# Kernel optimization log

Hardware: AMD Instinct MI355X
Metric: run time of the kernel (lower is better)

The kernel has to match this reference:

```python
import jax, jax.numpy as jnp
import numpy as np

B, D, U = 8192, 2048, 2048  # batch rows, input dim, units
NB_FACTOR = 3
MASK_DENSITY = 1.0 / 16.0  # butterfly-like sparse factor density


def _glorot_uniform(key, shape):
    fan_in, fan_out = shape[0], shape[-1]
    limit = np.sqrt(6.0 / (fan_in + fan_out)).astype(np.float32)
    return jax.random.uniform(key, shape, jnp.float32, -limit, limit)


def setup_inputs() -> dict:
    key = jax.random.key(0)
    kx, km0, km1, km2, kk0, kk1, kk2, ks = jax.random.split(key, 8)
    x = jax.random.normal(kx, (B, D), jnp.float32)
    # Fixed sparsity patterns (constants, like K.constant sparsity_masks)
    m0 = (jax.random.uniform(km0, (D, U)) < MASK_DENSITY).astype(jnp.float32)
    m1 = (jax.random.uniform(km1, (U, U)) < MASK_DENSITY).astype(jnp.float32)
    m2 = (jax.random.uniform(km2, (U, U)) < MASK_DENSITY).astype(jnp.float32)
    k0 = _glorot_uniform(kk0, (D, U))
    k1 = _glorot_uniform(kk1, (U, U))
    k2 = _glorot_uniform(kk2, (U, U))
    scaling = _glorot_uniform(ks, (1,))  # scaler weight, shape (1,)
    bias = jnp.zeros((U,), jnp.float32)
    return {"x": x, "k0": k0, "k1": k1, "k2": k2,
            "m0": m0, "m1": m1, "m2": m2,
            "scaling": scaling, "bias": bias}


def reference(x, k0, k1, k2, m0, m1, m2, scaling, bias):
    # output = activation(scaling * (x @ (k0*m0) @ (k1*m1) @ (k2*m2)) + bias)
    out = x @ (k0 * m0)          # [B, U]
    out = out @ (k1 * m1)        # [B, U]
    out = out @ (k2 * m2)        # [B, U]
    out = scaling * out + bias   # scale then channels-last bias add
    return jax.nn.relu(out)
```

## Files before the change

### kernel.cpp

```cpp
#include <hip/hip_runtime.h>
#include <hip/hip_bf16.h>


typedef __attribute__((ext_vector_type(8))) short  short8;
typedef __attribute__((ext_vector_type(8))) ushort ushort8v;
typedef __attribute__((ext_vector_type(4))) float  f32x4;

#define KD 2048
#define ND 2048

__device__ __forceinline__ ushort f2b(float f) {
    union { float f; unsigned u; } v; v.f = f;
    unsigned r = v.u + 0x7fffu + ((v.u >> 16) & 1u);
    return (ushort)(r >> 16);
}

__device__ __forceinline__ void gload16(const ushort* g, ushort* l) {
    __builtin_amdgcn_global_load_lds(
        (const __attribute__((address_space(1))) void*)g,
        (__attribute__((address_space(3))) void*)l, 16, 0, 0);
}

__global__ __launch_bounds__(256)
void convx(const float* __restrict__ x, ushort* __restrict__ xb)
{
    const size_t i = (size_t)blockIdx.x * 256 + threadIdx.x;
    const float4* src = reinterpret_cast<const float4*>(x) + i * 2;
    const float4 f0 = src[0], f1 = src[1];
    ushort8v u;
    u[0]=f2b(f0.x); u[1]=f2b(f0.y); u[2]=f2b(f0.z); u[3]=f2b(f0.w);
    u[4]=f2b(f1.x); u[5]=f2b(f1.y); u[6]=f2b(f1.z); u[7]=f2b(f1.w);
    reinterpret_cast<ushort8v*>(xb)[i] = u;
}

__global__ __launch_bounds__(256)
void convT3(const float* __restrict__ k0w, const float* __restrict__ k1w,
            const float* __restrict__ k2w, const float* __restrict__ m0w,
            const float* __restrict__ m1w, const float* __restrict__ m2w,
            ushort* __restrict__ wbT)
{
    const int z = blockIdx.z;
    const float* kw = z == 0 ? k0w : (z == 1 ? k1w : k2w);
    const float* mw = z == 0 ? m0w : (z == 1 ? m1w : m2w);
    ushort* o = wbT + (size_t)z * KD * ND;

    __shared__ ushort t[32][36];
    const int tid = threadIdx.x;
    const int bk = blockIdx.x * 32, bn = blockIdx.y * 32;
    {
        const int r = tid >> 3, c = (tid & 7) * 4;
        const size_t g = (size_t)(bk + r) * ND + bn + c;
        const float4 kv = *reinterpret_cast<const float4*>(kw + g);
        const float4 mv = *reinterpret_cast<const float4*>(mw + g);
        t[r][c + 0] = f2b(kv.x * mv.x);
        t[r][c + 1] = f2b(kv.y * mv.y);
        t[r][c + 2] = f2b(kv.z * mv.z);
        t[r][c + 3] = f2b(kv.w * mv.w);
    }
    __syncthreads();
    {
        const int n = tid >> 3, kq = (tid & 7) * 4;
        ushort4 ov;
        ov.x = t[kq + 0][n]; ov.y = t[kq + 1][n];
        ov.z = t[kq + 2][n]; ov.w = t[kq + 3][n];
        *reinterpret_cast<ushort4*>(&o[(size_t)(bn + n) * KD + bk + kq]) = ov;
    }
}

template<int EPI>
__global__ __launch_bounds__(512, 2)
void gemm256(const ushort* __restrict__ A, const ushort* __restrict__ BT,
             void* __restrict__ Cout,
             const float* __restrict__ scaling, const float* __restrict__ bias)
{
    __shared__ ushort S[2][2][2][256 * 32];

    const int tid  = threadIdx.x;
    const int lane = tid & 63;
    const int wid  = tid >> 6;
    const int wr   = wid >> 2, wc = wid & 3;
    const int l15  = lane & 15;
    const int kq   = lane >> 4;
    const int id   = blockIdx.x;
    const int swz  = (id & 7) * 32 + (id >> 3);
    const int bn   = (swz & 7) * 256;
    const int bm   = (swz >> 3) * 256;
    const int srow = lane >> 2;
    const int wrow = wid * 32;
    const int ssw  = ((lane & 3) ^ ((srow >> 1) & 3)) * 8;
    const int rsw  = (kq ^ ((l15 >> 1) & 3)) * 8;

    f32x4 acc[8][4] = {};

#define STAGE(op, bufl, kh, tile, G, g0) do {                                        \
    gload16(G + (size_t)((g0) + wrow + srow)      * KD + (tile)*64 + (kh)*32 + ssw,  \
            &S[bufl][op][kh][(wrow)      * 32]);                                     \
    gload16(G + (size_t)((g0) + wrow + 16 + srow) * KD + (tile)*64 + (kh)*32 + ssw,  \
            &S[bufl][op][kh][(wrow + 16) * 32]);                                     \
  } while (0)

#define BAR()  asm volatile("s_barrier" ::: "memory")
#define VM6()  asm volatile("s_waitcnt vmcnt(6)" ::: "memory")
#define VM0()  asm volatile("s_waitcnt vmcnt(0)" ::: "memory")
#define LGK0() asm volatile("s_waitcnt lgkmcnt(0)" ::: "memory")
#define SB()   __builtin_amdgcn_sched_barrier(0)
#define PRI1() __builtin_amdgcn_s_setprio(1)
#define PRI0() __builtin_amdgcn_s_setprio(0)

#define FA(bufl, kh, m) (*(const short8*)&S[bufl][0][kh][(wr*128 + (m)*16 + l15)*32 + rsw])
#define FB(bufl, kh, n) (*(const short8*)&S[bufl][1][kh][(wc*64  + (n)*16 + l15)*32 + rsw])

#define MM4(r, av, b0_, b1_, b2_, b3_)                                                \
    acc[r][0] = __builtin_amdgcn_mfma_f32_16x16x32_bf16(b0_, av, acc[r][0], 0, 0, 0); \
    acc[r][1] = __builtin_amdgcn_mfma_f32_16x16x32_bf16(b1_, av, acc[r][1], 0, 0, 0); \
    acc[r][2] = __builtin_amdgcn_mfma_f32_16x16x32_bf16(b2_, av, acc[r][2], 0, 0, 0); \
    acc[r][3] = __builtin_amdgcn_mfma_f32_16x16x32_bf16(b3_, av, acc[r][3], 0, 0, 0)

#define HALFGRP(bufl, ST0, ST1, ST2, ST3, GATE) do {                                  \
    short8 xa0 = FA(bufl,0,0), xa1 = FA(bufl,0,1), xa2 = FA(bufl,0,2), xa3 = FA(bufl,0,3); \
    short8 xb0 = FB(bufl,0,0), xb1 = FB(bufl,0,1), xb2 = FB(bufl,0,2), xb3 = FB(bufl,0,3); \
    ST0; BAR(); SB(); PRI1();                                                         \
    MM4(0, xa0, xb0, xb1, xb2, xb3); MM4(1, xa1, xb0, xb1, xb2, xb3);                 \
    MM4(2, xa2, xb0, xb1, xb2, xb3); MM4(3, xa3, xb0, xb1, xb2, xb3);                 \
    PRI0(); SB(); LGK0(); BAR();                                                      \
    short8 xa4 = FA(bufl,0,4), xa5 = FA(bufl,0,5), xa6 = FA(bufl,0,6), xa7 = FA(bufl,0,7); \
    short8 xc0 = FA(bufl,1,0), xc1 = FA(bufl,1,1), xc2 = FA(bufl,1,2), xc3 = FA(bufl,1,3); \
    ST1; BAR(); SB(); PRI1();                                                         \
    MM4(4, xa4, xb0, xb1, xb2, xb3); MM4(5, xa5, xb0, xb1, xb2, xb3);                 \
    MM4(6, xa6, xb0, xb1, xb2, xb3); MM4(7, xa7, xb0, xb1, xb2, xb3);                 \
    PRI0(); SB(); LGK0(); BAR();                                                      \
    short8 xc4 = FA(bufl,1,4), xc5 = FA(bufl,1,5), xc6 = FA(bufl,1,6), xc7 = FA(bufl,1,7); \
    short8 xd0 = FB(bufl,1,0), xd1 = FB(bufl,1,1), xd2 = FB(bufl,1,2), xd3 = FB(bufl,1,3); \
    ST2; BAR(); SB(); PRI1();                                                         \
    MM4(0, xc0, xd0, xd1, xd2, xd3); MM4(1, xc1, xd0, xd1, xd2, xd3);                 \
    MM4(2, xc2, xd0, xd1, xd2, xd3); MM4(3, xc3, xd0, xd1, xd2, xd3);                 \
    PRI0(); SB(); LGK0(); BAR();                                                      \
    ST3; GATE; BAR(); SB(); PRI1();                                                   \
    MM4(4, xc4, xd0, xd1, xd2, xd3); MM4(5, xc5, xd0, xd1, xd2, xd3);                 \
    MM4(6, xc6, xd0, xd1, xd2, xd3); MM4(7, xc7, xd0, xd1, xd2, xd3);                 \
    PRI0(); SB(); LGK0(); BAR();                                                      \
  } while (0)

    STAGE(0, 0, 0, 0, A,  bm); STAGE(0, 0, 1, 0, A,  bm);
    STAGE(1, 0, 0, 0, BT, bn); STAGE(1, 0, 1, 0, BT, bn);
    STAGE(1, 1, 0, 1, BT, bn); STAGE(0, 1, 0, 1, A,  bm); STAGE(0, 1, 1, 1, A,  bm);
    VM6();
    BAR();

    const int NITER = KD / 128;
    for (int it = 0; it < NITER - 1; ++it) {
        const int t1 = 2 * it + 1, t2 = 2 * it + 2, t3 = 2 * it + 3;
        HALFGRP(0,
                STAGE(1, 1, 1, t1, BT, bn),
                STAGE(1, 0, 0, t2, BT, bn),
                STAGE(0, 0, 0, t2, A,  bm),
                STAGE(0, 0, 1, t2, A,  bm),
                VM6());
        HALFGRP(1,
                STAGE(1, 0, 1, t2, BT, bn),
                STAGE(1, 1, 0, t3, BT, bn),
                STAGE(0, 1, 0, t3, A,  bm),
                STAGE(0, 1, 1, t3, A,  bm),
                VM6());
    }
    HALFGRP(0, STAGE(1, 1, 1, (KD / 64) - 1, BT, bn), , , , VM0());
    HALFGRP(1, , , , , );

    const float sc = EPI ? scaling[0] : 0.f;
#pragma unroll
    for (int m = 0; m < 8; ++m) {
        const size_t grow = (size_t)(bm + wr * 128 + m * 16 + l15);
#pragma unroll
        for (int n = 0; n < 4; ++n) {
            const int gcol = bn + wc * 64 + n * 16 + kq * 4;
            if constexpr (EPI) {
                const float4 bv = *reinterpret_cast<const float4*>(bias + gcol);
                float4 v;
                v.x = fmaxf(fmaf(sc, acc[m][n][0], bv.x), 0.f);
                v.y = fmaxf(fmaf(sc, acc[m][n][1], bv.y), 0.f);
                v.z = fmaxf(fmaf(sc, acc[m][n][2], bv.z), 0.f);
                v.w = fmaxf(fmaf(sc, acc[m][n][3], bv.w), 0.f);
                *reinterpret_cast<float4*>((float*)Cout + grow * ND + gcol) = v;
            } else {
                ushort4 v;
                v.x = f2b(acc[m][n][0]); v.y = f2b(acc[m][n][1]);
                v.z = f2b(acc[m][n][2]); v.w = f2b(acc[m][n][3]);
                *reinterpret_cast<ushort4*>((ushort*)Cout + grow * ND + gcol) = v;
            }
        }
    }
#undef STAGE
#undef HALFGRP
#undef MM4
#undef FA
#undef FB
}

extern "C" void kernel_launch(void* const* d_in, const int* in_sizes, int n_in,
                              void* d_out, int out_size, void* d_ws, size_t ws_size,
                              hipStream_t stream)
{
    const float* x    = (const float*)d_in[0];
    const float* k0w  = (const float*)d_in[1];
    const float* k1w  = (const float*)d_in[2];
    const float* k2w  = (const float*)d_in[3];
    const float* m0w  = (const float*)d_in[4];
    const float* m1w  = (const float*)d_in[5];
    const float* m2w  = (const float*)d_in[6];
    const float* sc   = (const float*)d_in[7];
    const float* bias = (const float*)d_in[8];

    const int Md = in_sizes[0] / KD;
    const size_t NE = (size_t)Md * KD;

    ushort* act1 = (ushort*)d_out;
    ushort* xb   = (ushort*)d_out + NE;
    float*  out  = (float*)d_out;
    ushort* act2 = (ushort*)d_ws;
    ushort* wbT  = (ushort*)d_ws + NE;

    dim3 bl(256);
    dim3 gX(NE / (256 * 8));
    dim3 gT(KD / 32, ND / 32, 3);
    dim3 gG((ND / 256) * (Md / 256)), bG(512);

    convx <<<gX, bl, 0, stream>>>(x, xb);
    convT3<<<gT, bl, 0, stream>>>(k0w, k1w, k2w, m0w, m1w, m2w, wbT);

    gemm256<0><<<gG, bG, 0, stream>>>(xb,   wbT,                     act1, nullptr, nullptr);
    gemm256<0><<<gG, bG, 0, stream>>>(act1, wbT + (size_t)KD * ND,     act2, nullptr, nullptr);
    gemm256<1><<<gG, bG, 0, stream>>>(act2, wbT + (size_t)2 * KD * ND, out,  sc, bias);
}
```

Baseline: 218.7 us.

## Switch GEMM to 32x32x16 MFMA tiles with four-phase K-half pipeline

```diff
diff --git a/kernel.cpp b/kernel.cpp
--- a/kernel.cpp
+++ b/kernel.cpp
@@ -2,9 +2,9 @@
 #include <hip/hip_bf16.h>
 
 
-typedef __attribute__((ext_vector_type(8))) short  short8;
-typedef __attribute__((ext_vector_type(8))) ushort ushort8v;
-typedef __attribute__((ext_vector_type(4))) float  f32x4;
+typedef __attribute__((ext_vector_type(8)))  short  short8;
+typedef __attribute__((ext_vector_type(8)))  ushort ushort8v;
+typedef __attribute__((ext_vector_type(16))) float  f32x16;
 
 #define KD 2048
 #define ND 2048
@@ -79,8 +79,9 @@
     const int lane = tid & 63;
     const int wid  = tid >> 6;
     const int wr   = wid >> 2, wc = wid & 3;
-    const int l15  = lane & 15;
-    const int kq   = lane >> 4;
+    const int l31  = lane & 31;
+    const int lh   = lane >> 5;
+    const int rk   = (l31 >> 1) & 3;
     const int id   = blockIdx.x;
     const int swz  = (id & 7) * 32 + (id >> 3);
     const int bn   = (swz & 7) * 256;
@@ -88,9 +89,8 @@
     const int srow = lane >> 2;
     const int wrow = wid * 32;
     const int ssw  = ((lane & 3) ^ ((srow >> 1) & 3)) * 8;
-    const int rsw  = (kq ^ ((l15 >> 1) & 3)) * 8;
-
-    f32x4 acc[8][4] = {};
+
+    f32x16 acc[4][2] = {};
 
 #define STAGE(op, bufl, kh, tile, G, g0) do {                                        \
     gload16(G + (size_t)((g0) + wrow + srow)      * KD + (tile)*64 + (kh)*32 + ssw,  \
@@ -100,100 +100,89 @@
   } while (0)
 
 #define BAR()  asm volatile("s_barrier" ::: "memory")
-#define VM6()  asm volatile("s_waitcnt vmcnt(6)" ::: "memory")
+#define VM4()  asm volatile("s_waitcnt vmcnt(4)" ::: "memory")
 #define VM0()  asm volatile("s_waitcnt vmcnt(0)" ::: "memory")
 #define LGK0() asm volatile("s_waitcnt lgkmcnt(0)" ::: "memory")
 #define SB()   __builtin_amdgcn_sched_barrier(0)
 #define PRI1() __builtin_amdgcn_s_setprio(1)
 #define PRI0() __builtin_amdgcn_s_setprio(0)
 
-#define FA(bufl, kh, m) (*(const short8*)&S[bufl][0][kh][(wr*128 + (m)*16 + l15)*32 + rsw])
-#define FB(bufl, kh, n) (*(const short8*)&S[bufl][1][kh][(wc*64  + (n)*16 + l15)*32 + rsw])
-
-#define MM4(r, av, b0_, b1_, b2_, b3_)                                                \
-    acc[r][0] = __builtin_amdgcn_mfma_f32_16x16x32_bf16(b0_, av, acc[r][0], 0, 0, 0); \
-    acc[r][1] = __builtin_amdgcn_mfma_f32_16x16x32_bf16(b1_, av, acc[r][1], 0, 0, 0); \
-    acc[r][2] = __builtin_amdgcn_mfma_f32_16x16x32_bf16(b2_, av, acc[r][2], 0, 0, 0); \
-    acc[r][3] = __builtin_amdgcn_mfma_f32_16x16x32_bf16(b3_, av, acc[r][3], 0, 0, 0)
-
-#define HALFGRP(bufl, ST0, ST1, ST2, ST3, GATE) do {                                  \
-    short8 xa0 = FA(bufl,0,0), xa1 = FA(bufl,0,1), xa2 = FA(bufl,0,2), xa3 = FA(bufl,0,3); \
-    short8 xb0 = FB(bufl,0,0), xb1 = FB(bufl,0,1), xb2 = FB(bufl,0,2), xb3 = FB(bufl,0,3); \
-    ST0; BAR(); SB(); PRI1();                                                         \
-    MM4(0, xa0, xb0, xb1, xb2, xb3); MM4(1, xa1, xb0, xb1, xb2, xb3);                 \
-    MM4(2, xa2, xb0, xb1, xb2, xb3); MM4(3, xa3, xb0, xb1, xb2, xb3);                 \
-    PRI0(); SB(); LGK0(); BAR();                                                      \
-    short8 xa4 = FA(bufl,0,4), xa5 = FA(bufl,0,5), xa6 = FA(bufl,0,6), xa7 = FA(bufl,0,7); \
-    short8 xc0 = FA(bufl,1,0), xc1 = FA(bufl,1,1), xc2 = FA(bufl,1,2), xc3 = FA(bufl,1,3); \
-    ST1; BAR(); SB(); PRI1();                                                         \
-    MM4(4, xa4, xb0, xb1, xb2, xb3); MM4(5, xa5, xb0, xb1, xb2, xb3);                 \
-    MM4(6, xa6, xb0, xb1, xb2, xb3); MM4(7, xa7, xb0, xb1, xb2, xb3);                 \
-    PRI0(); SB(); LGK0(); BAR();                                                      \
-    short8 xc4 = FA(bufl,1,4), xc5 = FA(bufl,1,5), xc6 = FA(bufl,1,6), xc7 = FA(bufl,1,7); \
-    short8 xd0 = FB(bufl,1,0), xd1 = FB(bufl,1,1), xd2 = FB(bufl,1,2), xd3 = FB(bufl,1,3); \
-    ST2; BAR(); SB(); PRI1();                                                         \
-    MM4(0, xc0, xd0, xd1, xd2, xd3); MM4(1, xc1, xd0, xd1, xd2, xd3);                 \
-    MM4(2, xc2, xd0, xd1, xd2, xd3); MM4(3, xc3, xd0, xd1, xd2, xd3);                 \
-    PRI0(); SB(); LGK0(); BAR();                                                      \
-    ST3; GATE; BAR(); SB(); PRI1();                                                   \
-    MM4(4, xc4, xd0, xd1, xd2, xd3); MM4(5, xc5, xd0, xd1, xd2, xd3);                 \
-    MM4(6, xc6, xd0, xd1, xd2, xd3); MM4(7, xc7, xd0, xd1, xd2, xd3);                 \
-    PRI0(); SB(); LGK0(); BAR();                                                      \
+#define FA32(bufl, kh, mt, ks) (*(const short8*)&S[bufl][0][kh][ \
+        (wr*128 + (mt)*32 + l31)*32 + ((((ks)*2 + lh) ^ rk) * 8)])
+#define FB32(bufl, kh, nt, ks) (*(const short8*)&S[bufl][1][kh][ \
+        (wc*64  + (nt)*32 + l31)*32 + ((((ks)*2 + lh) ^ rk) * 8)])
+
+#define MF(a_, b_, c_) __builtin_amdgcn_mfma_f32_32x32x16_bf16(a_, b_, c_, 0, 0, 0)
+
+#define PH(bufl, kh, STG, GATE) do {                                                  \
+    short8 a00=FA32(bufl,kh,0,0), a10=FA32(bufl,kh,1,0),                              \
+           a20=FA32(bufl,kh,2,0), a30=FA32(bufl,kh,3,0);                              \
+    short8 a01=FA32(bufl,kh,0,1), a11=FA32(bufl,kh,1,1),                              \
+           a21=FA32(bufl,kh,2,1), a31=FA32(bufl,kh,3,1);                              \
+    short8 b00=FB32(bufl,kh,0,0), b10=FB32(bufl,kh,1,0);                              \
+    short8 b01=FB32(bufl,kh,0,1), b11=FB32(bufl,kh,1,1);                              \
+    STG; BAR(); SB(); PRI1();                                                         \
+    acc[0][0]=MF(b00,a00,acc[0][0]); acc[1][0]=MF(b00,a10,acc[1][0]);                 \
+    acc[2][0]=MF(b00,a20,acc[2][0]); acc[3][0]=MF(b00,a30,acc[3][0]);                 \
+    acc[0][1]=MF(b10,a00,acc[0][1]); acc[1][1]=MF(b10,a10,acc[1][1]);                 \
+    acc[2][1]=MF(b10,a20,acc[2][1]); acc[3][1]=MF(b10,a30,acc[3][1]);                 \
+    acc[0][0]=MF(b01,a01,acc[0][0]); acc[1][0]=MF(b01,a11,acc[1][0]);                 \
+    acc[2][0]=MF(b01,a21,acc[2][0]); acc[3][0]=MF(b01,a31,acc[3][0]);                 \
+    acc[0][1]=MF(b11,a01,acc[0][1]); acc[1][1]=MF(b11,a11,acc[1][1]);                 \
+    acc[2][1]=MF(b11,a21,acc[2][1]); acc[3][1]=MF(b11,a31,acc[3][1]);                 \
+    PRI0(); SB(); LGK0(); GATE; BAR();                                                \
   } while (0)
 
-    STAGE(0, 0, 0, 0, A,  bm); STAGE(0, 0, 1, 0, A,  bm);
-    STAGE(1, 0, 0, 0, BT, bn); STAGE(1, 0, 1, 0, BT, bn);
-    STAGE(1, 1, 0, 1, BT, bn); STAGE(0, 1, 0, 1, A,  bm); STAGE(0, 1, 1, 1, A,  bm);
-    VM6();
+    STAGE(0, 0, 0, 0, A,  bm); STAGE(1, 0, 0, 0, BT, bn);
+    STAGE(0, 0, 1, 0, A,  bm); STAGE(1, 0, 1, 0, BT, bn);
+    STAGE(1, 1, 0, 1, BT, bn); STAGE(0, 1, 0, 1, A,  bm);
+    VM4();
     BAR();
 
     const int NITER = KD / 128;
     for (int it = 0; it < NITER - 1; ++it) {
         const int t1 = 2 * it + 1, t2 = 2 * it + 2, t3 = 2 * it + 3;
-        HALFGRP(0,
-                STAGE(1, 1, 1, t1, BT, bn),
-                STAGE(1, 0, 0, t2, BT, bn),
-                STAGE(0, 0, 0, t2, A,  bm),
-                STAGE(0, 0, 1, t2, A,  bm),
-                VM6());
-        HALFGRP(1,
-                STAGE(1, 0, 1, t2, BT, bn),
-                STAGE(1, 1, 0, t3, BT, bn),
-                STAGE(0, 1, 0, t3, A,  bm),
-                STAGE(0, 1, 1, t3, A,  bm),
-                VM6());
-    }
-    HALFGRP(0, STAGE(1, 1, 1, (KD / 64) - 1, BT, bn), , , , VM0());
-    HALFGRP(1, , , , , );
+        PH(0, 0, STAGE(1,1,1,t1,BT,bn); STAGE(0,1,1,t1,A,bm), );
+        PH(0, 1, STAGE(1,0,0,t2,BT,bn); STAGE(0,0,0,t2,A,bm), VM4());
+        PH(1, 0, STAGE(1,0,1,t2,BT,bn); STAGE(0,0,1,t2,A,bm), );
+        PH(1, 1, STAGE(1,1,0,t3,BT,bn); STAGE(0,1,0,t3,A,bm), VM4());
+    }
+    PH(0, 0, STAGE(1,1,1,31,BT,bn); STAGE(0,1,1,31,A,bm), );
+    PH(0, 1, , VM0());
+    PH(1, 0, , );
+    PH(1, 1, , );
 
     const float sc = EPI ? scaling[0] : 0.f;
 #pragma unroll
-    for (int m = 0; m < 8; ++m) {
-        const size_t grow = (size_t)(bm + wr * 128 + m * 16 + l15);
+    for (int mt = 0; mt < 4; ++mt) {
+        const size_t grow = (size_t)(bm + wr * 128 + mt * 32 + l31);
 #pragma unroll
-        for (int n = 0; n < 4; ++n) {
-            const int gcol = bn + wc * 64 + n * 16 + kq * 4;
-            if constexpr (EPI) {
-                const float4 bv = *reinterpret_cast<const float4*>(bias + gcol);
-                float4 v;
-                v.x = fmaxf(fmaf(sc, acc[m][n][0], bv.x), 0.f);
-                v.y = fmaxf(fmaf(sc, acc[m][n][1], bv.y), 0.f);
-                v.z = fmaxf(fmaf(sc, acc[m][n][2], bv.z), 0.f);
-                v.w = fmaxf(fmaf(sc, acc[m][n][3], bv.w), 0.f);
-                *reinterpret_cast<float4*>((float*)Cout + grow * ND + gcol) = v;
-            } else {
-                ushort4 v;
-                v.x = f2b(acc[m][n][0]); v.y = f2b(acc[m][n][1]);
-                v.z = f2b(acc[m][n][2]); v.w = f2b(acc[m][n][3]);
-                *reinterpret_cast<ushort4*>((ushort*)Cout + grow * ND + gcol) = v;
+        for (int nt = 0; nt < 2; ++nt) {
+#pragma unroll
+            for (int r = 0; r < 4; ++r) {
+                const int gcol = bn + wc * 64 + nt * 32 + lh * 4 + r * 8;
+                if constexpr (EPI) {
+                    const float4 bv = *reinterpret_cast<const float4*>(bias + gcol);
+                    float4 v;
+                    v.x = fmaxf(fmaf(sc, acc[mt][nt][4*r+0], bv.x), 0.f);
+                    v.y = fmaxf(fmaf(sc, acc[mt][nt][4*r+1], bv.y), 0.f);
+                    v.z = fmaxf(fmaf(sc, acc[mt][nt][4*r+2], bv.z), 0.f);
+                    v.w = fmaxf(fmaf(sc, acc[mt][nt][4*r+3], bv.w), 0.f);
+                    *reinterpret_cast<float4*>((float*)Cout + grow * ND + gcol) = v;
+                } else {
+                    ushort4 v;
+                    v.x = f2b(acc[mt][nt][4*r+0]); v.y = f2b(acc[mt][nt][4*r+1]);
+                    v.z = f2b(acc[mt][nt][4*r+2]); v.w = f2b(acc[mt][nt][4*r+3]);
+                    *reinterpret_cast<ushort4*>((ushort*)Cout + grow * ND + gcol) = v;
+                }
             }
         }
     }
 #undef STAGE
-#undef HALFGRP
-#undef MM4
-#undef FA
-#undef FB
+#undef PH
+#undef MF
+#undef FA32
+#undef FB32
 }
 
 extern "C" void kernel_launch(void* const* d_in, const int* in_sizes, int n_in,
```

Measured after the change: 262.1 us. 1.2x slower.

## Restructure GEMM main loop into four k-half phases with paired A/B staging

Applied to the files above, without the earlier changes.

```diff
diff --git a/kernel.cpp b/kernel.cpp
--- a/kernel.cpp
+++ b/kernel.cpp
@@ -100,7 +100,7 @@
   } while (0)
 
 #define BAR()  asm volatile("s_barrier" ::: "memory")
-#define VM6()  asm volatile("s_waitcnt vmcnt(6)" ::: "memory")
+#define VM4()  asm volatile("s_waitcnt vmcnt(4)" ::: "memory")
 #define VM0()  asm volatile("s_waitcnt vmcnt(0)" ::: "memory")
 #define LGK0() asm volatile("s_waitcnt lgkmcnt(0)" ::: "memory")
 #define SB()   __builtin_amdgcn_sched_barrier(0)
@@ -110,61 +110,44 @@
 #define FA(bufl, kh, m) (*(const short8*)&S[bufl][0][kh][(wr*128 + (m)*16 + l15)*32 + rsw])
 #define FB(bufl, kh, n) (*(const short8*)&S[bufl][1][kh][(wc*64  + (n)*16 + l15)*32 + rsw])
 
-#define MM4(r, av, b0_, b1_, b2_, b3_)                                                \
-    acc[r][0] = __builtin_amdgcn_mfma_f32_16x16x32_bf16(b0_, av, acc[r][0], 0, 0, 0); \
-    acc[r][1] = __builtin_amdgcn_mfma_f32_16x16x32_bf16(b1_, av, acc[r][1], 0, 0, 0); \
-    acc[r][2] = __builtin_amdgcn_mfma_f32_16x16x32_bf16(b2_, av, acc[r][2], 0, 0, 0); \
-    acc[r][3] = __builtin_amdgcn_mfma_f32_16x16x32_bf16(b3_, av, acc[r][3], 0, 0, 0)
-
-#define HALFGRP(bufl, ST0, ST1, ST2, ST3, GATE) do {                                  \
-    short8 xa0 = FA(bufl,0,0), xa1 = FA(bufl,0,1), xa2 = FA(bufl,0,2), xa3 = FA(bufl,0,3); \
-    short8 xb0 = FB(bufl,0,0), xb1 = FB(bufl,0,1), xb2 = FB(bufl,0,2), xb3 = FB(bufl,0,3); \
-    ST0; BAR(); SB(); PRI1();                                                         \
-    MM4(0, xa0, xb0, xb1, xb2, xb3); MM4(1, xa1, xb0, xb1, xb2, xb3);                 \
-    MM4(2, xa2, xb0, xb1, xb2, xb3); MM4(3, xa3, xb0, xb1, xb2, xb3);                 \
-    PRI0(); SB(); LGK0(); BAR();                                                      \
-    short8 xa4 = FA(bufl,0,4), xa5 = FA(bufl,0,5), xa6 = FA(bufl,0,6), xa7 = FA(bufl,0,7); \
-    short8 xc0 = FA(bufl,1,0), xc1 = FA(bufl,1,1), xc2 = FA(bufl,1,2), xc3 = FA(bufl,1,3); \
-    ST1; BAR(); SB(); PRI1();                                                         \
-    MM4(4, xa4, xb0, xb1, xb2, xb3); MM4(5, xa5, xb0, xb1, xb2, xb3);                 \
-    MM4(6, xa6, xb0, xb1, xb2, xb3); MM4(7, xa7, xb0, xb1, xb2, xb3);                 \
-    PRI0(); SB(); LGK0(); BAR();                                                      \
-    short8 xc4 = FA(bufl,1,4), xc5 = FA(bufl,1,5), xc6 = FA(bufl,1,6), xc7 = FA(bufl,1,7); \
-    short8 xd0 = FB(bufl,1,0), xd1 = FB(bufl,1,1), xd2 = FB(bufl,1,2), xd3 = FB(bufl,1,3); \
-    ST2; BAR(); SB(); PRI1();                                                         \
-    MM4(0, xc0, xd0, xd1, xd2, xd3); MM4(1, xc1, xd0, xd1, xd2, xd3);                 \
-    MM4(2, xc2, xd0, xd1, xd2, xd3); MM4(3, xc3, xd0, xd1, xd2, xd3);                 \
-    PRI0(); SB(); LGK0(); BAR();                                                      \
-    ST3; GATE; BAR(); SB(); PRI1();                                                   \
-    MM4(4, xc4, xd0, xd1, xd2, xd3); MM4(5, xc5, xd0, xd1, xd2, xd3);                 \
-    MM4(6, xc6, xd0, xd1, xd2, xd3); MM4(7, xc7, xd0, xd1, xd2, xd3);                 \
-    PRI0(); SB(); LGK0(); BAR();                                                      \
+#define MF(a_, b_, c_) __builtin_amdgcn_mfma_f32_16x16x32_bf16(a_, b_, c_, 0, 0, 0)
+
+#define MMROW(m, am)                                     \
+    acc[m][0] = MF(bf0, am, acc[m][0]);                  \
+    acc[m][1] = MF(bf1, am, acc[m][1]);                  \
+    acc[m][2] = MF(bf2, am, acc[m][2]);                  \
+    acc[m][3] = MF(bf3, am, acc[m][3])
+
+#define PH(bufl, kh, STG, GATE) do {                                                  \
+    short8 af0 = FA(bufl,kh,0), af1 = FA(bufl,kh,1), af2 = FA(bufl,kh,2),             \
+           af3 = FA(bufl,kh,3), af4 = FA(bufl,kh,4), af5 = FA(bufl,kh,5),             \
+           af6 = FA(bufl,kh,6), af7 = FA(bufl,kh,7);                                  \
+    short8 bf0 = FB(bufl,kh,0), bf1 = FB(bufl,kh,1),                                  \
+           bf2 = FB(bufl,kh,2), bf3 = FB(bufl,kh,3);                                  \
+    STG; BAR(); SB(); PRI1();                                                         \
+    MMROW(0, af0); MMROW(1, af1); MMROW(2, af2); MMROW(3, af3);                       \
+    MMROW(4, af4); MMROW(5, af5); MMROW(6, af6); MMROW(7, af7);                       \
+    PRI0(); SB(); LGK0(); GATE; BAR();                                                \
   } while (0)
 
-    STAGE(0, 0, 0, 0, A,  bm); STAGE(0, 0, 1, 0, A,  bm);
-    STAGE(1, 0, 0, 0, BT, bn); STAGE(1, 0, 1, 0, BT, bn);
-    STAGE(1, 1, 0, 1, BT, bn); STAGE(0, 1, 0, 1, A,  bm); STAGE(0, 1, 1, 1, A,  bm);
-    VM6();
+    STAGE(0, 0, 0, 0, A,  bm); STAGE(1, 0, 0, 0, BT, bn);
+    STAGE(0, 0, 1, 0, A,  bm); STAGE(1, 0, 1, 0, BT, bn);
+    STAGE(1, 1, 0, 1, BT, bn); STAGE(0, 1, 0, 1, A,  bm);
+    VM4();
     BAR();
 
     const int NITER = KD / 128;
     for (int it = 0; it < NITER - 1; ++it) {
-        const int t1 = 2 * it + 1, t2 = 2 * it + 2, t3 = 2 * it + 3;
-        HALFGRP(0,
-                STAGE(1, 1, 1, t1, BT, bn),
-                STAGE(1, 0, 0, t2, BT, bn),
-                STAGE(0, 0, 0, t2, A,  bm),
-                STAGE(0, 0, 1, t2, A,  bm),
-                VM6());
-        HALFGRP(1,
-                STAGE(1, 0, 1, t2, BT, bn),
-                STAGE(1, 1, 0, t3, BT, bn),
-                STAGE(0, 1, 0, t3, A,  bm),
-                STAGE(0, 1, 1, t3, A,  bm),
-                VM6());
-    }
-    HALFGRP(0, STAGE(1, 1, 1, (KD / 64) - 1, BT, bn), , , , VM0());
-    HALFGRP(1, , , , , );
+        const int t2 = 2 * it + 2, t3 = 2 * it + 3;
+        PH(0, 0, STAGE(1,1,1,t3-2,BT,bn); STAGE(0,1,1,t3-2,A,bm), );
+        PH(0, 1, STAGE(1,0,0,t2,BT,bn);   STAGE(0,0,0,t2,A,bm),   VM4());
+        PH(1, 0, STAGE(1,0,1,t2,BT,bn);   STAGE(0,0,1,t2,A,bm),   );
+        PH(1, 1, STAGE(1,1,0,t3,BT,bn);   STAGE(0,1,0,t3,A,bm),   VM4());
+    }
+    PH(0, 0, STAGE(1,1,1,31,BT,bn); STAGE(0,1,1,31,A,bm), );
+    PH(0, 1, , VM0());
+    PH(1, 0, , );
+    PH(1, 1, , );
 
     const float sc = EPI ? scaling[0] : 0.f;
 #pragma unroll
@@ -190,8 +173,9 @@
         }
     }
 #undef STAGE
-#undef HALFGRP
-#undef MM4
+#undef PH
+#undef MF
+#undef MMROW
 #undef FA
 #undef FB
 }
```

Measured after the change: 225.3 us. +3.0%, slower.
